# Performance work log

Measured on AMD Instinct MI355X. Metric: run time of the kernel, lower is better.

Reference implementation:

```python
import jax, jax.numpy as jnp
import numpy as np

D = 1024
NUM_HEADS = 16
HEAD_SIZE = D // NUM_HEADS  # scaling factor only; no actual head split in original

def setup_inputs() -> dict:
    key = jax.random.key(0)
    ks = jax.random.split(key, 9)
    B, S = 4, 2048
    inp = {
        'incorporacao': jax.random.normal(ks[0], (B, S, D), dtype=jnp.float32),
        'Wq': jax.random.normal(ks[1], (D, D), dtype=jnp.float32) * (1.0 / np.sqrt(D)),
        'bq': jnp.zeros((D,), dtype=jnp.float32),
        'Wk': jax.random.normal(ks[2], (D, D), dtype=jnp.float32) * (1.0 / np.sqrt(D)),
        'bk': jnp.zeros((D,), dtype=jnp.float32),
        'Wv': jax.random.normal(ks[3], (D, D), dtype=jnp.float32) * (1.0 / np.sqrt(D)),
        'bv': jnp.zeros((D,), dtype=jnp.float32),
        'Wo': jax.random.normal(ks[4], (D, D), dtype=jnp.float32) * (1.0 / np.sqrt(D)),
        'bo': jnp.zeros((D,), dtype=jnp.float32),
    }
    return inp

def reference(incorporacao, Wq, bq, Wk, bk, Wv, bv, Wo, bo):
    # Faithful to original: NO head split; attention over full embedding dim,
    # scaled by sqrt(head_size) = sqrt(D / num_cabecas).
    q = jnp.einsum('bsd,df->bsf', incorporacao, Wq) + bq  # [B,S,D]
    k = jnp.einsum('bsd,df->bsf', incorporacao, Wk) + bk
    v = jnp.einsum('bsd,df->bsf', incorporacao, Wv) + bv
    scores = jnp.einsum('bsd,btd->bst', q, k) / jnp.sqrt(jnp.float32(HEAD_SIZE))  # [B,S,S]
    attn = jax.nn.softmax(scores, axis=-1)
    ctx = jnp.einsum('bst,btd->bsd', attn, v)  # [B,S,D]
    out = jnp.einsum('bsd,df->bsf', ctx, Wo) + bo
    return out
```

## Files before the change

### kernel.cpp

```cpp
#include <hip/hip_runtime.h>
#include <cstdint>
#include <cstddef>

typedef unsigned short u16;
typedef __attribute__((ext_vector_type(8))) short short8;
typedef __attribute__((ext_vector_type(4))) float f32x4;

#define BB 4
#define SS 2048
#define DD 1024

__device__ __forceinline__ u16 f2bf(float f) {
  union { float f; unsigned u; } x; x.f = f;
  unsigned r = x.u + 0x7FFFu + ((x.u >> 16) & 1u);
  return (u16)(r >> 16);
}

__device__ __forceinline__ void gld_lds16(const void* g, void* l) {
  __builtin_amdgcn_global_load_lds(
      (const __attribute__((address_space(1))) void*)g,
      (__attribute__((address_space(3))) void*)l, 16, 0, 0);
}

__device__ __forceinline__ void store_out(float* p, float v) { *p = v; }
__device__ __forceinline__ void store_out(u16* p, float v) { *p = f2bf(v); }

template<typename OutT, int MODE, bool HAS_BIAS>
__global__ __launch_bounds__(512, 1) void gemm1b(
    const u16* __restrict__ A, size_t sA, int ldaB,
    const u16* __restrict__ B, size_t sB, int ldbB,
    OutT* __restrict__ C, size_t sC, int ldc,
    const float* __restrict__ bias, float scale, int K,
    u16* __restrict__ out2, u16* __restrict__ out3)
{
  constexpr int SLOT = 24576;
  __shared__ u16 sm[3 * SLOT];

  const int gx = gridDim.x, gy = gridDim.y;
  const int nwg = gx * gy * gridDim.z;
  const int flat = blockIdx.x + gx * (blockIdx.y + gy * blockIdx.z);
  const int swz = (flat & 7) * (nwg >> 3) + (flat >> 3);
  const int bz  = swz / (gx * gy);
  const int rem = swz - bz * (gx * gy);
  const int by  = rem / gx;
  const int bx  = rem - by * gx;
  const int blockM = by * 128, blockN = bx * 256;

  const char* Abase = (const char*)(A + (size_t)bz * sA);
  const char* Bbase = (const char*)(B + (size_t)bz * sB);

  const int tid  = threadIdx.x;
  const int wave = tid >> 6, lane = tid & 63;
  const int wrow = (wave >> 2) * 64;
  const int wcol = (wave & 3) * 64;

  const int sr  = tid >> 2;
  const int scb = ((tid & 3) * 16) ^ (((sr >> 1) & 3) << 4);
  const char* gA0 = Abase + (size_t)(blockM + sr)       * ldaB + scb;
  const char* gB0 = Bbase + (size_t)(blockN + sr)       * ldbB + scb;
  const char* gB1 = Bbase + (size_t)(blockN + sr + 128) * ldbB + scb;
  const int ldsw = wave * 512;

  auto STG1 = [&](u16* S, int t1) {
    const int kb = t1 * 128;
    gld_lds16(gA0 + kb,      S + ldsw);
    gld_lds16(gA0 + kb + 64, S + 4096 + ldsw);
    gld_lds16(gB0 + kb,      S + 8192 + ldsw);
  };
  auto STG2 = [&](u16* S, int t1) {
    const int kb = t1 * 128;
    gld_lds16(gB1 + kb,      S + 12288 + ldsw);
    gld_lds16(gB0 + kb + 64, S + 16384 + ldsw);
    gld_lds16(gB1 + kb + 64, S + 20480 + ldsw);
  };

  const int r16 = lane & 15, q8 = (lane >> 4) * 8;
  int offA[4], offB[4];
#pragma unroll
  for (int mi = 0; mi < 4; ++mi) {
    const int row = wrow + mi * 16 + r16;
    offA[mi] = row * 32 + (q8 ^ (((row >> 1) & 3) << 3));
  }
#pragma unroll
  for (int nj = 0; nj < 4; ++nj) {
    const int row = wcol + nj * 16 + r16;
    offB[nj] = row * 32 + (q8 ^ (((row >> 1) & 3) << 3));
  }

  f32x4 acc[4][4] = {};
  const bool vblk = (MODE == 1) && (blockN >= 2048);

  auto MMA = [&](short8* a2, short8* b2) {
    __builtin_amdgcn_s_setprio(1);
    if (vblk) {
#pragma unroll
      for (int mi = 0; mi < 4; ++mi)
#pragma unroll
        for (int nj = 0; nj < 4; ++nj)
          acc[mi][nj] = __builtin_amdgcn_mfma_f32_16x16x32_bf16(
              b2[nj], a2[mi], acc[mi][nj], 0, 0, 0);
    } else {
#pragma unroll
      for (int mi = 0; mi < 4; ++mi)
#pragma unroll
        for (int nj = 0; nj < 4; ++nj)
          acc[mi][nj] = __builtin_amdgcn_mfma_f32_16x16x32_bf16(
              a2[mi], b2[nj], acc[mi][nj], 0, 0, 0);
    }
    __builtin_amdgcn_s_setprio(0);
  };

  const int NT = K >> 6;

  u16* S0 = sm;
  u16* S1 = sm + SLOT;
  u16* S2 = sm + 2 * SLOT;

  STG1(S0, 0); STG2(S0, 0);
  STG1(S1, 1); STG2(S1, 1);

  short8 a[4], b[4];
  for (int t = 0; t < NT; ++t) {
    if (t + 1 < NT) asm volatile("s_waitcnt vmcnt(6)" ::: "memory");
    else            asm volatile("s_waitcnt vmcnt(0)" ::: "memory");
    __builtin_amdgcn_s_barrier();
    __builtin_amdgcn_sched_barrier(0);

    const bool more = (t + 2 < NT);

#pragma unroll
    for (int nj = 0; nj < 4; ++nj) b[nj] = *(const short8*)(S0 + 8192 + offB[nj]);
#pragma unroll
    for (int mi = 0; mi < 4; ++mi) a[mi] = *(const short8*)(S0 + offA[mi]);
    if (more) STG1(S2, t + 2);
    MMA(a, b);

#pragma unroll
    for (int nj = 0; nj < 4; ++nj) b[nj] = *(const short8*)(S0 + 16384 + offB[nj]);
#pragma unroll
    for (int mi = 0; mi < 4; ++mi) a[mi] = *(const short8*)(S0 + 4096 + offA[mi]);
    if (more) STG2(S2, t + 2);
    MMA(a, b);

    u16* tmp = S0; S0 = S1; S1 = S2; S2 = tmp;
  }

  const int cr = lane & 15, rr0 = (lane >> 4) * 4;
  OutT* Cb = C + (size_t)bz * sC;
  if (vblk) {
#pragma unroll
    for (int nj = 0; nj < 4; ++nj) {
#pragma unroll
      for (int mi = 0; mi < 4; ++mi) {
        f32x4 v = acc[mi][nj];
        const int tg = blockM + wrow + mi * 16 + cr;
        const int b_ = tg >> 11, t0 = tg & 2047;
        const int d0 = blockN - 2048 + wcol + nj * 16 + rr0;
#pragma unroll
        for (int i = 0; i < 4; ++i) {
          const float bval = HAS_BIAS ? bias[2048 + d0 + i] : 0.0f;
          out3[((size_t)b_ * 1024 + d0 + i) * 2048 + t0] = f2bf(v[i] + bval);
        }
      }
    }
  } else {
#pragma unroll
    for (int nj = 0; nj < 4; ++nj) {
      const int colg = blockN + wcol + nj * 16 + cr;
      const float bval = HAS_BIAS ? bias[colg] : 0.0f;
#pragma unroll
      for (int mi = 0; mi < 4; ++mi) {
        f32x4 v = acc[mi][nj];
        const int rowg = blockM + wrow + mi * 16 + rr0;
        if constexpr (MODE == 0) {
#pragma unroll
          for (int i = 0; i < 4; ++i)
            store_out(&Cb[(size_t)(rowg + i) * ldc + colg], v[i] * scale + bval);
        } else {
          u16* dst = (colg < 1024) ? (u16*)Cb : out2;
          const int c2 = colg & 1023;
#pragma unroll
          for (int i = 0; i < 4; ++i)
            dst[(size_t)(rowg + i) * 1024 + c2] = f2bf(v[i] + bval);
        }
      }
    }
  }
}

__global__ __launch_bounds__(256) void cvt_f32_bf16(
    const float* __restrict__ in, u16* __restrict__ out, int n4)
{
  int i = blockIdx.x * 256 + threadIdx.x;
  if (i >= n4) return;
  float4 v = ((const float4*)in)[i];
  uint2 u;
  u.x = (unsigned)f2bf(v.x) | ((unsigned)f2bf(v.y) << 16);
  u.y = (unsigned)f2bf(v.z) | ((unsigned)f2bf(v.w) << 16);
  ((uint2*)out)[i] = u;
}

__global__ __launch_bounds__(256) void transpose_cvt(
    const float* __restrict__ W, u16* __restrict__ Wt)
{
  __shared__ u16 tile[32][33];
  const int tx = threadIdx.x;
  const int ty = threadIdx.y;
  const int bx = blockIdx.x * 32;
  const int by = blockIdx.y * 32;
#pragma unroll
  for (int j = 0; j < 4; ++j) {
    int d = by + ty * 4 + j;
    tile[ty * 4 + j][tx] = f2bf(W[(size_t)d * DD + bx + tx]);
  }
  __syncthreads();
#pragma unroll
  for (int j = 0; j < 4; ++j) {
    int f = bx + ty * 4 + j;
    Wt[(size_t)f * DD + by + tx] = tile[tx][ty * 4 + j];
  }
}

__global__ __launch_bounds__(256) void concat_bias(
    const float* __restrict__ bq, const float* __restrict__ bk,
    const float* __restrict__ bv, float* __restrict__ out)
{
  int i = blockIdx.x * 256 + threadIdx.x;
  const float* src = (i < 1024) ? bq : ((i < 2048) ? bk : bv);
  out[i] = src[i & 1023];
}

__global__ __launch_bounds__(256) void softmax_inplace(float* __restrict__ S)
{
  const int tid = threadIdx.x;
  float* rp = S + (size_t)blockIdx.x * SS;

  float4 v0 = ((const float4*)rp)[tid];
  float4 v1 = ((const float4*)rp)[tid + 256];

  float m = fmaxf(fmaxf(fmaxf(v0.x, v0.y), fmaxf(v0.z, v0.w)),
                  fmaxf(fmaxf(v1.x, v1.y), fmaxf(v1.z, v1.w)));
#pragma unroll
  for (int off = 32; off; off >>= 1) m = fmaxf(m, __shfl_xor(m, off));

  __shared__ float smax[4];
  __shared__ float ssum[4];
  const int wave = tid >> 6, lane = tid & 63;
  if (lane == 0) smax[wave] = m;
  __syncthreads();
  m = fmaxf(fmaxf(smax[0], smax[1]), fmaxf(smax[2], smax[3]));

  float e[8];
  e[0] = __expf(v0.x - m); e[1] = __expf(v0.y - m);
  e[2] = __expf(v0.z - m); e[3] = __expf(v0.w - m);
  e[4] = __expf(v1.x - m); e[5] = __expf(v1.y - m);
  e[6] = __expf(v1.z - m); e[7] = __expf(v1.w - m);
  float s = e[0] + e[1] + e[2] + e[3] + e[4] + e[5] + e[6] + e[7];
#pragma unroll
  for (int off = 32; off; off >>= 1) s += __shfl_xor(s, off);
  if (lane == 0) ssum[wave] = s;
  __syncthreads();
  float inv = 1.0f / (ssum[0] + ssum[1] + ssum[2] + ssum[3]);

  uint2 u0, u1;
  u0.x = (unsigned)f2bf(e[0] * inv) | ((unsigned)f2bf(e[1] * inv) << 16);
  u0.y = (unsigned)f2bf(e[2] * inv) | ((unsigned)f2bf(e[3] * inv) << 16);
  u1.x = (unsigned)f2bf(e[4] * inv) | ((unsigned)f2bf(e[5] * inv) << 16);
  u1.y = (unsigned)f2bf(e[6] * inv) | ((unsigned)f2bf(e[7] * inv) << 16);
  ((uint2*)rp)[tid]       = u0;
  ((uint2*)rp)[tid + 256] = u1;
}

extern "C" void kernel_launch(void* const* d_in, const int* in_sizes, int n_in,
                              void* d_out, int out_size, void* d_ws, size_t ws_size,
                              hipStream_t stream) {
  (void)in_sizes; (void)n_in; (void)out_size; (void)ws_size;
  const float* X  = (const float*)d_in[0];
  const float* Wq = (const float*)d_in[1];
  const float* bq = (const float*)d_in[2];
  const float* Wk = (const float*)d_in[3];
  const float* bk = (const float*)d_in[4];
  const float* Wv = (const float*)d_in[5];
  const float* bv = (const float*)d_in[6];
  const float* Wo = (const float*)d_in[7];
  const float* bo = (const float*)d_in[8];

  char* ws = (char*)d_ws;
  const size_t MBy = 1ull << 20;
  u16*   Xbf   = (u16*)(ws + 0);
  u16*   WtAll = (u16*)(ws + 16 * MBy);
  u16*   Wto   = (u16*)(ws + 22 * MBy);
  u16*   Qb    = (u16*)(ws + 24 * MBy);
  u16*   Kb    = (u16*)(ws + 40 * MBy);
  u16*   Vt    = (u16*)(ws + 56 * MBy);
  float* Sf    = (float*)(ws + 72 * MBy);
  float* bqkv  = (float*)(ws + 72 * MBy);
  u16*   Ctx   = (u16*)(ws + 136 * MBy);

  cvt_f32_bf16<<<dim3((BB * SS * DD / 4) / 256), 256, 0, stream>>>(X, Xbf, BB * SS * DD / 4);
  dim3 tb(32, 8);
  transpose_cvt<<<dim3(32, 32), tb, 0, stream>>>(Wq, WtAll);
  transpose_cvt<<<dim3(32, 32), tb, 0, stream>>>(Wk, WtAll + 1024 * 1024);
  transpose_cvt<<<dim3(32, 32), tb, 0, stream>>>(Wv, WtAll + 2 * 1024 * 1024);
  transpose_cvt<<<dim3(32, 32), tb, 0, stream>>>(Wo, Wto);
  concat_bias<<<dim3(12), 256, 0, stream>>>(bq, bk, bv, bqkv);

  gemm1b<u16, 1, true><<<dim3(12, 64, 1), 512, 0, stream>>>(
      Xbf, 0, DD * 2, WtAll, 0, DD * 2,
      Qb, 0, 0, bqkv, 1.0f, DD, Kb, Vt);

  gemm1b<float, 0, false><<<dim3(8, 16, BB), 512, 0, stream>>>(
      Qb, (size_t)SS * DD, DD * 2, Kb, (size_t)SS * DD, DD * 2,
      Sf, (size_t)SS * SS, SS, nullptr, 0.125f, DD, nullptr, nullptr);

  softmax_inplace<<<dim3(BB * SS), 256, 0, stream>>>(Sf);

  gemm1b<u16, 0, false><<<dim3(4, 16, BB), 512, 0, stream>>>(
      (const u16*)Sf, (size_t)SS * 2 * SS, 2 * SS * 2,
      Vt, (size_t)DD * SS, SS * 2,
      Ctx, (size_t)SS * DD, DD, nullptr, 1.0f, SS, nullptr, nullptr);

  gemm1b<float, 0, true><<<dim3(4, 64, 1), 512, 0, stream>>>(
      Ctx, 0, DD * 2, Wto, 0, DD * 2,
      (float*)d_out, 0, DD, bo, 1.0f, DD, nullptr, nullptr);
}
```

Baseline: 196.3 us.

## Add 256x256-tile double-buffered GEMM kernel for QKV projection and scores

Adds a new GEMM kernel, gemm2b, that computes 256x256 output tiles with 8 waves. Each wave owns a 128x64 sub-tile, and the kernel double-buffers 64-wide K slices in LDS, staging A and B separately in between MFMA halves. The kernel is used for the fused QKV projection and the QK^T scores GEMM, which halves the number of workgroups and raises operand reuse per LDS load. In exchange, each wave holds more accumulator registers, the grid becomes coarser with possible tail imbalance, and there is one fewer pipeline stage than the 3-slot gemm1b.

Result: slower. 428.4 us (+118.3%).

```diff
diff --git a/kernel.cpp b/kernel.cpp
--- a/kernel.cpp
+++ b/kernel.cpp
@@ -24,6 +24,178 @@
 
 __device__ __forceinline__ void store_out(float* p, float v) { *p = v; }
 __device__ __forceinline__ void store_out(u16* p, float v) { *p = f2bf(v); }
+
+template<typename OutT, int MODE, bool HAS_BIAS>
+__global__ __launch_bounds__(512, 1) void gemm2b(
+    const u16* __restrict__ A, size_t sA, int ldaB,
+    const u16* __restrict__ B, size_t sB, int ldbB,
+    OutT* __restrict__ C, size_t sC, int ldc,
+    const float* __restrict__ bias, float scale, int K,
+    u16* __restrict__ out2, u16* __restrict__ out3)
+{
+  __shared__ u16 sm[2 * 32768];
+
+  const int gx = gridDim.x, gy = gridDim.y;
+  const int nwg = gx * gy * gridDim.z;
+  const int flat = blockIdx.x + gx * (blockIdx.y + gy * blockIdx.z);
+  const int swz = (flat & 7) * (nwg >> 3) + (flat >> 3);
+  const int bz  = swz / (gx * gy);
+  const int rem = swz - bz * (gx * gy);
+  const int by  = rem / gx;
+  const int bx  = rem - by * gx;
+  const int blockM = by * 256, blockN = bx * 256;
+
+  const char* Abase = (const char*)(A + (size_t)bz * sA);
+  const char* Bbase = (const char*)(B + (size_t)bz * sB);
+
+  const int tid  = threadIdx.x;
+  const int wave = tid >> 6, lane = tid & 63;
+  const int wrow = (wave >> 2) * 128;
+  const int wcol = (wave & 3) * 64;
+
+  const int sr  = tid >> 3;
+  const int scb = ((tid & 7) * 16) ^ ((sr & 7) << 4);
+  const char* gAs = Abase + (size_t)(blockM + sr) * ldaB + scb;
+  const char* gBs = Bbase + (size_t)(blockN + sr) * ldbB + scb;
+
+  auto STG_A = [&](int t1) {
+    u16* D = sm + (t1 & 1) * 32768 + wave * 512;
+    const int kb = t1 * 128;
+    gld_lds16(gAs + kb,                          D);
+    gld_lds16(gAs + kb + (size_t)64  * ldaB,     D + 4096);
+    gld_lds16(gAs + kb + (size_t)128 * ldaB,     D + 8192);
+    gld_lds16(gAs + kb + (size_t)192 * ldaB,     D + 12288);
+  };
+  auto STG_B = [&](int t1) {
+    u16* D = sm + (t1 & 1) * 32768 + 16384 + wave * 512;
+    const int kb = t1 * 128;
+    gld_lds16(gBs + kb,                          D);
+    gld_lds16(gBs + kb + (size_t)64  * ldbB,     D + 4096);
+    gld_lds16(gBs + kb + (size_t)128 * ldbB,     D + 8192);
+    gld_lds16(gBs + kb + (size_t)192 * ldbB,     D + 12288);
+  };
+
+  const int r16 = lane & 15, q = lane >> 4;
+  int offA[8], offB[4];
+#pragma unroll
+  for (int mi = 0; mi < 8; ++mi) {
+    const int row = wrow + mi * 16 + r16;
+    offA[mi] = row * 64 + 8 * (q ^ (row & 7));
+  }
+#pragma unroll
+  for (int nj = 0; nj < 4; ++nj) {
+    const int row = wcol + nj * 16 + r16;
+    offB[nj] = row * 64 + 8 * (q ^ (row & 7));
+  }
+
+  f32x4 acc[8][4] = {};
+  const bool vblk = (MODE == 1) && (blockN >= 2048);
+
+  const int NT = K >> 6;
+
+  STG_A(0); STG_B(0);
+  STG_A(1); STG_B(1);
+
+  for (int t = 0; t < NT; ++t) {
+    if (t == 0) asm volatile("s_waitcnt vmcnt(8)" ::: "memory");
+    else        asm volatile("s_waitcnt vmcnt(0)" ::: "memory");
+    __builtin_amdgcn_s_barrier();
+    __builtin_amdgcn_sched_barrier(0);
+
+    const u16* Ap = sm + (t & 1) * 32768;
+    const u16* Bp = Ap + 16384;
+    const bool stg = (t >= 1) && (t + 1 < NT);
+
+    short8 a[8], b[4];
+#pragma unroll
+    for (int nj = 0; nj < 4; ++nj) b[nj] = *(const short8*)(Bp + offB[nj]);
+#pragma unroll
+    for (int mi = 0; mi < 8; ++mi) a[mi] = *(const short8*)(Ap + offA[mi]);
+    if (stg) STG_A(t + 1);
+    __builtin_amdgcn_s_setprio(1);
+    if (vblk) {
+#pragma unroll
+      for (int mi = 0; mi < 8; ++mi)
+#pragma unroll
+        for (int nj = 0; nj < 4; ++nj)
+          acc[mi][nj] = __builtin_amdgcn_mfma_f32_16x16x32_bf16(
+              b[nj], a[mi], acc[mi][nj], 0, 0, 0);
+    } else {
+#pragma unroll
+      for (int mi = 0; mi < 8; ++mi)
+#pragma unroll
+        for (int nj = 0; nj < 4; ++nj)
+          acc[mi][nj] = __builtin_amdgcn_mfma_f32_16x16x32_bf16(
+              a[mi], b[nj], acc[mi][nj], 0, 0, 0);
+    }
+    __builtin_amdgcn_s_setprio(0);
+
+#pragma unroll
+    for (int nj = 0; nj < 4; ++nj) b[nj] = *(const short8*)(Bp + (offB[nj] ^ 32));
+#pragma unroll
+    for (int mi = 0; mi < 8; ++mi) a[mi] = *(const short8*)(Ap + (offA[mi] ^ 32));
+    if (stg) STG_B(t + 1);
+    __builtin_amdgcn_s_setprio(1);
+    if (vblk) {
+#pragma unroll
+      for (int mi = 0; mi < 8; ++mi)
+#pragma unroll
+        for (int nj = 0; nj < 4; ++nj)
+          acc[mi][nj] = __builtin_amdgcn_mfma_f32_16x16x32_bf16(
+              b[nj], a[mi], acc[mi][nj], 0, 0, 0);
+    } else {
+#pragma unroll
+      for (int mi = 0; mi < 8; ++mi)
+#pragma unroll
+        for (int nj = 0; nj < 4; ++nj)
+          acc[mi][nj] = __builtin_amdgcn_mfma_f32_16x16x32_bf16(
+              a[mi], b[nj], acc[mi][nj], 0, 0, 0);
+    }
+    __builtin_amdgcn_s_setprio(0);
+  }
+
+  const int cr = lane & 15, rr0 = (lane >> 4) * 4;
+  OutT* Cb = C + (size_t)bz * sC;
+  if (vblk) {
+#pragma unroll
+    for (int nj = 0; nj < 4; ++nj) {
+#pragma unroll
+      for (int mi = 0; mi < 8; ++mi) {
+        f32x4 v = acc[mi][nj];
+        const int tg = blockM + wrow + mi * 16 + cr;
+        const int b_ = tg >> 11, t0 = tg & 2047;
+        const int d0 = blockN - 2048 + wcol + nj * 16 + rr0;
+#pragma unroll
+        for (int i = 0; i < 4; ++i) {
+          const float bval = HAS_BIAS ? bias[2048 + d0 + i] : 0.0f;
+          out3[((size_t)b_ * 1024 + d0 + i) * 2048 + t0] = f2bf(v[i] + bval);
+        }
+      }
+    }
+  } else {
+#pragma unroll
+    for (int nj = 0; nj < 4; ++nj) {
+      const int colg = blockN + wcol + nj * 16 + cr;
+      const float bval = HAS_BIAS ? bias[colg] : 0.0f;
+#pragma unroll
+      for (int mi = 0; mi < 8; ++mi) {
+        f32x4 v = acc[mi][nj];
+        const int rowg = blockM + wrow + mi * 16 + rr0;
+        if constexpr (MODE == 0) {
+#pragma unroll
+          for (int i = 0; i < 4; ++i)
+            store_out(&Cb[(size_t)(rowg + i) * ldc + colg], v[i] * scale + bval);
+        } else {
+          u16* dst = (colg < 1024) ? (u16*)Cb : out2;
+          const int c2 = colg & 1023;
+#pragma unroll
+          for (int i = 0; i < 4; ++i)
+            dst[(size_t)(rowg + i) * 1024 + c2] = f2bf(v[i] + bval);
+        }
+      }
+    }
+  }
+}
 
 template<typename OutT, int MODE, bool HAS_BIAS>
 __global__ __launch_bounds__(512, 1) void gemm1b(
@@ -305,11 +477,11 @@
   transpose_cvt<<<dim3(32, 32), tb, 0, stream>>>(Wo, Wto);
   concat_bias<<<dim3(12), 256, 0, stream>>>(bq, bk, bv, bqkv);
 
-  gemm1b<u16, 1, true><<<dim3(12, 64, 1), 512, 0, stream>>>(
+  gemm2b<u16, 1, true><<<dim3(12, 32, 1), 512, 0, stream>>>(
       Xbf, 0, DD * 2, WtAll, 0, DD * 2,
       Qb, 0, 0, bqkv, 1.0f, DD, Kb, Vt);
 
-  gemm1b<float, 0, false><<<dim3(8, 16, BB), 512, 0, stream>>>(
+  gemm2b<float, 0, false><<<dim3(8, 8, BB), 512, 0, stream>>>(
       Qb, (size_t)SS * DD, DD * 2, Kb, (size_t)SS * DD, DD * 2,
       Sf, (size_t)SS * SS, SS, nullptr, 0.125f, DD, nullptr, nullptr);
 
```
